# Performance work log

Measured on AMD Instinct MI355X. Metric: run time of the kernel, lower is better.

Reference implementation:

```python
import jax, jax.numpy as jnp
import numpy as np

N, E = 50000, 600000
D_IN, D_H, D_OUT, D_E = 128, 128, 128, 32


def setup_inputs() -> dict:
    key = jax.random.key(0)
    ks = jax.random.split(key, 20)
    s = 0.05
    inp = {
        "x": jax.random.normal(ks[0], (N, D_IN), dtype=jnp.float32),
        "edge_index": jax.random.randint(ks[1], (2, E), 0, N, dtype=jnp.int64),
        "edge_attr": jax.random.normal(ks[2], (E, D_E), dtype=jnp.float32),
        # layer 0 (GINEConv MLP + edge lin: edge_dim -> in_channels)
        "w1_0": jax.random.normal(ks[3], (D_IN, D_H), dtype=jnp.float32) * s,
        "b1_0": jnp.zeros((D_H,), jnp.float32),
        "w2_0": jax.random.normal(ks[4], (D_H, D_H), dtype=jnp.float32) * s,
        "b2_0": jnp.zeros((D_H,), jnp.float32),
        "we_0": jax.random.normal(ks[5], (D_E, D_IN), dtype=jnp.float32) * s,
        "be_0": jnp.zeros((D_IN,), jnp.float32),
        # layer 1 (edge lin: edge_dim -> hidden_channels)
        "w1_1": jax.random.normal(ks[6], (D_H, D_H), dtype=jnp.float32) * s,
        "b1_1": jnp.zeros((D_H,), jnp.float32),
        "w2_1": jax.random.normal(ks[7], (D_H, D_H), dtype=jnp.float32) * s,
        "b2_1": jnp.zeros((D_H,), jnp.float32),
        "we_1": jax.random.normal(ks[8], (D_E, D_H), dtype=jnp.float32) * s,
        "be_1": jnp.zeros((D_H,), jnp.float32),
        # output head
        "fc1_w": jax.random.normal(ks[9], (D_H, D_H), dtype=jnp.float32) * s,
        "fc1_b": jnp.zeros((D_H,), jnp.float32),
        "fc2_w": jax.random.normal(ks[10], (D_H, D_OUT), dtype=jnp.float32) * s,
        "fc2_b": jnp.zeros((D_OUT,), jnp.float32),
    }
    return inp


def _gine_layer(x, src, dst, edge_attr, we, be, w1, b1, w2, b2):
    # GINEConv (eps=0): out = MLP(x + sum_j ReLU(x_j + edge_lin(e_ij)))
    e_emb = edge_attr @ we + be                       # [E, d]
    msg = jax.nn.relu(x[src] + e_emb)                 # gather + message
    agg = jax.ops.segment_sum(msg, dst, num_segments=x.shape[0])  # scatter-add
    h = agg + x                                       # (1 + eps) * x, eps = 0
    return jnp.maximum(h @ w1 + b1, 0.0) @ w2 + b2    # 2-layer MLP


def reference(x, edge_index, edge_attr,
              w1_0, b1_0, w2_0, b2_0, we_0, be_0,
              w1_1, b1_1, w2_1, b2_1, we_1, be_1,
              fc1_w, fc1_b, fc2_w, fc2_b):
    src, dst = edge_index[0], edge_index[1]
    h = _gine_layer(x, src, dst, edge_attr, we_0, be_0, w1_0, b1_0, w2_0, b2_0)
    h = jax.nn.relu(h)  # activation (dropout=0 -> identity)
    h = _gine_layer(h, src, dst, edge_attr, we_1, be_1, w1_1, b1_1, w2_1, b2_1)
    h = jax.nn.relu(h)
    h = jax.nn.relu(h @ fc1_w + fc1_b)
    return h @ fc2_w + fc2_b
```

## Files before the change

kernel.cpp:

```cpp
#include <hip/hip_runtime.h>
#include <stdint.h>


#define ND 128
#define ED 32

typedef __attribute__((ext_vector_type(8))) short short8;
typedef __attribute__((ext_vector_type(4))) float f32x4;

__device__ inline unsigned short bf16_hi(float f) {
    union { float f; unsigned u; } v;
    v.f = f;
    return (unsigned short)(v.u >> 16);
}
__device__ inline float bf16_f(unsigned short h) {
    union { unsigned u; float f; } v;
    v.u = ((unsigned)h) << 16;
    return v.f;
}

__global__ __launch_bounds__(256) void zero_kernel(int* __restrict__ p, int n) {
    int i = blockIdx.x * blockDim.x + threadIdx.x;
    if (i < n) p[i] = 0;
}

__global__ __launch_bounds__(256) void hist_kernel(const int* __restrict__ ei,
                                                   int* __restrict__ counts, int E) {
    int i = blockIdx.x * blockDim.x + threadIdx.x;
    if (i < E) atomicAdd(&counts[ei[E + i]], 1);
}

__global__ __launch_bounds__(256) void bsum_kernel(const int* __restrict__ counts,
                                                   int* __restrict__ bsum, int N) {
    __shared__ int s[256];
    int t = threadIdx.x;
    int i = blockIdx.x * 256 + t;
    s[t] = (i < N) ? counts[i] : 0;
    __syncthreads();
#pragma unroll
    for (int off = 128; off > 0; off >>= 1) {
        if (t < off) s[t] += s[t + off];
        __syncthreads();
    }
    if (t == 0) bsum[blockIdx.x] = s[0];
}

__global__ __launch_bounds__(256) void scan_bsums(const int* __restrict__ bsum,
                                                  int* __restrict__ bofs,
                                                  int* __restrict__ row_start_N, int NB) {
    __shared__ int s[256];
    int t = threadIdx.x;
    int chunk = (NB + 255) >> 8;
    int lo = min(t * chunk, NB);
    int hi = min(lo + chunk, NB);
    int sum = 0;
    for (int i = lo; i < hi; ++i) sum += bsum[i];
    s[t] = sum;
    __syncthreads();
    for (int off = 1; off < 256; off <<= 1) {
        int v = (t >= off) ? s[t - off] : 0;
        __syncthreads();
        s[t] += v;
        __syncthreads();
    }
    int pre = (t == 0) ? 0 : s[t - 1];
    for (int i = lo; i < hi; ++i) {
        bofs[i] = pre;
        pre += bsum[i];
    }
    if (t == 255) *row_start_N = s[255];
}

__global__ __launch_bounds__(256) void expand_kernel(const int* __restrict__ counts,
                                                     const int* __restrict__ bofs,
                                                     int* __restrict__ row_start,
                                                     int* __restrict__ woff, int N) {
    __shared__ int s[256];
    int t = threadIdx.x;
    int i = blockIdx.x * 256 + t;
    int c = (i < N) ? counts[i] : 0;
    s[t] = c;
    __syncthreads();
    for (int off = 1; off < 256; off <<= 1) {
        int v = (t >= off) ? s[t - off] : 0;
        __syncthreads();
        s[t] += v;
        __syncthreads();
    }
    if (i < N) {
        int pre = bofs[blockIdx.x] + s[t] - c;
        row_start[i] = pre;
        woff[i] = pre;
    }
}

__global__ __launch_bounds__(256) void scatter_kernel(const int* __restrict__ ei,
                                                      int* __restrict__ woff,
                                                      int2* __restrict__ pack, int E) {
    int i = blockIdx.x * blockDim.x + threadIdx.x;
    if (i < E) {
        int d = ei[E + i];
        int p = atomicAdd(&woff[d], 1);
        pack[p] = make_int2(ei[i], i);
    }
}

__global__ __launch_bounds__(256) void wprep_kernel(
    const float* __restrict__ w0, const float* __restrict__ w1,
    const float* __restrict__ w2, const float* __restrict__ w3,
    const float* __restrict__ w4, const float* __restrict__ w5,
    unsigned short* __restrict__ hi, unsigned short* __restrict__ lo) {
    int t = blockIdx.x * blockDim.x + threadIdx.x;
    const float* W;
    switch (blockIdx.y) {
        case 0: W = w0; break;
        case 1: W = w1; break;
        case 2: W = w2; break;
        case 3: W = w3; break;
        case 4: W = w4; break;
        default: W = w5; break;
    }
    unsigned short* dh = hi + (size_t)blockIdx.y * 16384;
    unsigned short* dl = lo + (size_t)blockIdx.y * 16384;
    int c = t >> 6, l = t & 63;
    int nt = c >> 2, ks = c & 3;
    int n = nt * 16 + (l & 15);
    int kb = ks * 32 + ((l >> 4) << 3);
#pragma unroll
    for (int j = 0; j < 8; ++j) {
        float f = W[(size_t)(kb + j) * ND + n];
        unsigned short h = bf16_hi(f);
        dh[((size_t)c * 64 + l) * 8 + j] = h;
        dl[((size_t)c * 64 + l) * 8 + j] = bf16_hi(f - bf16_f(h));
    }
}

__global__ __launch_bounds__(256) void wprep_we(const float* __restrict__ w0,
                                                const float* __restrict__ w1,
                                                unsigned short* __restrict__ hi) {
    int t = threadIdx.x;
    int c = (blockIdx.x << 2) + (t >> 6);
    int l = t & 63;
    const float* W = blockIdx.y ? w1 : w0;
    unsigned short* dh = hi + (size_t)blockIdx.y * 4096;
    int n = c * 16 + (l & 15);
    int kb = (l >> 4) << 3;
#pragma unroll
    for (int j = 0; j < 8; ++j)
        dh[((size_t)c * 64 + l) * 8 + j] = bf16_hi(W[(size_t)(kb + j) * ND + n]);
}

__global__ __launch_bounds__(256) void xprep_kernel(const float* __restrict__ X,
                                                    const float* __restrict__ be,
                                                    unsigned short* __restrict__ xpk,
                                                    int N) {
    int t = blockIdx.x * 256 + threadIdx.x;
    int total = (N + 1) * 16;
    if (t >= total) return;
    int v = t >> 4, g = t & 15;
    short8 h, l;
    if (v < N) {
        const float4* p = (const float4*)(X + (size_t)v * ND + g * 8);
        float4 a0 = p[0], a1 = p[1];
        float f[8] = {a0.x, a0.y, a0.z, a0.w, a1.x, a1.y, a1.z, a1.w};
#pragma unroll
        for (int j = 0; j < 8; ++j) {
            float fv = f[j] + be[g * 8 + j];
            unsigned short hh = bf16_hi(fv);
            h[j] = (short)hh;
            l[j] = (short)bf16_hi(fv - bf16_f(hh));
        }
    } else {
#pragma unroll
        for (int j = 0; j < 8; ++j) {
            h[j] = (short)0xC6EA;
            l[j] = 0;
        }
    }
    unsigned short* dst = xpk + (size_t)t * 16;
    *(short8*)dst = h;
    *(short8*)(dst + 8) = l;
}

__global__ __launch_bounds__(256, 4) void agg_mfma(
    const float* __restrict__ xin, const float* __restrict__ edge_attr,
    const unsigned short* __restrict__ xpk, const unsigned short* __restrict__ bfh,
    const int* __restrict__ row_start, const int2* __restrict__ pack,
    float* __restrict__ hout, int N, int NW) {
    int lane = threadIdx.x & 63;
    int gw = (blockIdx.x * blockDim.x + threadIdx.x) >> 6;
    int m = lane & 15;
    int quad = lane >> 4;

    short8 bh[8];
#pragma unroll
    for (int nt = 0; nt < 8; ++nt)
        bh[nt] = *(const short8*)(bfh + ((size_t)nt * 64 + lane) * 8);

    short8 idf[2];
#pragma unroll
    for (int q = 0; q < 2; ++q)
#pragma unroll
        for (int j = 0; j < 8; ++j)
            idf[q][j] = (quad * 8 + j == q * 16 + m) ? (short)0x3F80 : (short)0;

    int col0 = quad * 32 + m;
    int col1 = col0 + 16;

    for (int v = gw; v < N; v += NW) {
        int beg = row_start[v];
        int end = row_start[v + 1];
        float res0 = xin[(size_t)v * ND + col0];
        float res1 = xin[(size_t)v * ND + col1];
        float part[8];
#pragma unroll
        for (int nt = 0; nt < 8; ++nt) part[nt] = 0.f;

        for (int base = beg; base < end; base += 16) {
            int rem = end - base;
            int mm = m < rem ? m : rem - 1;
            int2 pk = pack[base + mm];
            int s = m < rem ? pk.x : N;

            const unsigned short* xr = xpk + ((size_t)s * 16 + quad) * 16;
            short8 xh[4], xl[4];
#pragma unroll
            for (int kc = 0; kc < 4; ++kc) {
                xh[kc] = *(const short8*)(xr + kc * 64);
                xl[kc] = *(const short8*)(xr + kc * 64 + 8);
            }
            const float4* ar = (const float4*)(edge_attr + (size_t)pk.y * ED + quad * 8);
            float4 a0 = ar[0], a1 = ar[1];

            float af[8] = {a0.x, a0.y, a0.z, a0.w, a1.x, a1.y, a1.z, a1.w};
            short8 ah, al;
#pragma unroll
            for (int j = 0; j < 8; ++j) {
                unsigned short h = bf16_hi(af[j]);
                ah[j] = (short)h;
                al[j] = (short)bf16_hi(af[j] - bf16_f(h));
            }

#pragma unroll
            for (int nt = 0; nt < 8; ++nt) {
                f32x4 a = {0.f, 0.f, 0.f, 0.f};
                a = __builtin_amdgcn_mfma_f32_16x16x32_bf16(ah, bh[nt], a, 0, 0, 0);
                a = __builtin_amdgcn_mfma_f32_16x16x32_bf16(al, bh[nt], a, 0, 0, 0);
                a = __builtin_amdgcn_mfma_f32_16x16x32_bf16(xh[nt >> 1], idf[nt & 1], a,
                                                            0, 0, 0);
                a = __builtin_amdgcn_mfma_f32_16x16x32_bf16(xl[nt >> 1], idf[nt & 1], a,
                                                            0, 0, 0);
#pragma unroll
                for (int r = 0; r < 4; ++r)
                    part[nt] += fmaxf(a[r], 0.f);
            }
        }
#pragma unroll
        for (int nt = 0; nt < 8; ++nt) {
            float p = part[nt];
            p += __shfl_xor(p, 16, 64);
            p += __shfl_xor(p, 32, 64);
            part[nt] = p;
        }
        float o0 = quad == 0 ? part[0] : quad == 1 ? part[2] : quad == 2 ? part[4] : part[6];
        float o1 = quad == 0 ? part[1] : quad == 1 ? part[3] : quad == 2 ? part[5] : part[7];
        hout[(size_t)v * ND + col0] = res0 + o0;
        hout[(size_t)v * ND + col1] = res1 + o1;
    }
}

#define LP 132
__global__ __launch_bounds__(256, 4) void mlp2_mfma(
    const float* __restrict__ A,
    const unsigned short* __restrict__ w1h, const unsigned short* __restrict__ w1l,
    const float* __restrict__ b1,
    const unsigned short* __restrict__ w2h, const unsigned short* __restrict__ w2l,
    const float* __restrict__ b2,
    float* __restrict__ C, int N, int relu2) {
    __shared__ float tile[4][16 * LP];
    int lane = threadIdx.x & 63;
    int wave = threadIdx.x >> 6;
    int gw = blockIdx.x * 4 + wave;
    int m0 = gw * 16;
    if (m0 >= N) return;
    int m = lane & 15;
    int quad = lane >> 4;
    float* T = tile[wave];

    int row = m0 + m;
    bool rok = row < N;
    short8 ah[4], al[4];
#pragma unroll
    for (int ks = 0; ks < 4; ++ks) {
        float f[8];
        if (rok) {
            const float4* p = (const float4*)(A + (size_t)row * ND + ks * 32 + quad * 8);
            float4 a0 = p[0], a1 = p[1];
            f[0] = a0.x; f[1] = a0.y; f[2] = a0.z; f[3] = a0.w;
            f[4] = a1.x; f[5] = a1.y; f[6] = a1.z; f[7] = a1.w;
        } else {
#pragma unroll
            for (int j = 0; j < 8; ++j) f[j] = 0.f;
        }
#pragma unroll
        for (int j = 0; j < 8; ++j) {
            unsigned short hh = bf16_hi(f[j]);
            ah[ks][j] = (short)hh;
            al[ks][j] = (short)bf16_hi(f[j] - bf16_f(hh));
        }
    }

#pragma unroll
    for (int nt = 0; nt < 8; ++nt) {
        f32x4 acc = {0.f, 0.f, 0.f, 0.f};
#pragma unroll
        for (int ks = 0; ks < 4; ++ks) {
            size_t off = ((size_t)(nt * 4 + ks) * 64 + lane) * 8;
            short8 bh = *(const short8*)(w1h + off);
            short8 bl = *(const short8*)(w1l + off);
            acc = __builtin_amdgcn_mfma_f32_16x16x32_bf16(ah[ks], bh, acc, 0, 0, 0);
            acc = __builtin_amdgcn_mfma_f32_16x16x32_bf16(al[ks], bh, acc, 0, 0, 0);
            acc = __builtin_amdgcn_mfma_f32_16x16x32_bf16(ah[ks], bl, acc, 0, 0, 0);
        }
        float bv = b1[nt * 16 + m];
#pragma unroll
        for (int r = 0; r < 4; ++r) {
            float o = acc[r] + bv;
            o = o > 0.f ? o : 0.f;
            T[(quad * 4 + r) * LP + nt * 16 + m] = o;
        }
    }

    short8 ch[4], cl[4];
#pragma unroll
    for (int ks = 0; ks < 4; ++ks) {
        const float4* p = (const float4*)(T + m * LP + ks * 32 + quad * 8);
        float4 a0 = p[0], a1 = p[1];
        float f[8] = {a0.x, a0.y, a0.z, a0.w, a1.x, a1.y, a1.z, a1.w};
#pragma unroll
        for (int j = 0; j < 8; ++j) {
            unsigned short hh = bf16_hi(f[j]);
            ch[ks][j] = (short)hh;
            cl[ks][j] = (short)bf16_hi(f[j] - bf16_f(hh));
        }
    }

#pragma unroll
    for (int nt = 0; nt < 8; ++nt) {
        f32x4 acc = {0.f, 0.f, 0.f, 0.f};
#pragma unroll
        for (int ks = 0; ks < 4; ++ks) {
            size_t off = ((size_t)(nt * 4 + ks) * 64 + lane) * 8;
            short8 bh = *(const short8*)(w2h + off);
            short8 bl = *(const short8*)(w2l + off);
            acc = __builtin_amdgcn_mfma_f32_16x16x32_bf16(ch[ks], bh, acc, 0, 0, 0);
            acc = __builtin_amdgcn_mfma_f32_16x16x32_bf16(cl[ks], bh, acc, 0, 0, 0);
            acc = __builtin_amdgcn_mfma_f32_16x16x32_bf16(ch[ks], bl, acc, 0, 0, 0);
        }
        float bv = b2[nt * 16 + m];
#pragma unroll
        for (int r = 0; r < 4; ++r) {
            int rr = m0 + quad * 4 + r;
            if (rr < N) {
                float o = acc[r] + bv;
                if (relu2) o = o > 0.f ? o : 0.f;
                C[(size_t)rr * ND + nt * 16 + m] = o;
            }
        }
    }
}

extern "C" void kernel_launch(void* const* d_in, const int* in_sizes, int n_in,
                              void* d_out, int out_size, void* d_ws, size_t ws_size,
                              hipStream_t stream) {
    const float* x = (const float*)d_in[0];
    const int* ei = (const int*)d_in[1];
    const float* ea = (const float*)d_in[2];
    const float* w1_0 = (const float*)d_in[3];
    const float* b1_0 = (const float*)d_in[4];
    const float* w2_0 = (const float*)d_in[5];
    const float* b2_0 = (const float*)d_in[6];
    const float* we_0 = (const float*)d_in[7];
    const float* be_0 = (const float*)d_in[8];
    const float* w1_1 = (const float*)d_in[9];
    const float* b1_1 = (const float*)d_in[10];
    const float* w2_1 = (const float*)d_in[11];
    const float* b2_1 = (const float*)d_in[12];
    const float* we_1 = (const float*)d_in[13];
    const float* be_1 = (const float*)d_in[14];
    const float* fc1_w = (const float*)d_in[15];
    const float* fc1_b = (const float*)d_in[16];
    const float* fc2_w = (const float*)d_in[17];
    const float* fc2_b = (const float*)d_in[18];

    int N = in_sizes[0] / ND;
    int E = in_sizes[2] / ED;
    int NB = (N + 255) / 256;

    float* bufA = (float*)d_ws;
    int* counts = (int*)(bufA + (size_t)N * ND);
    int* row_start = counts + N;
    int* woff = row_start + (N + 1);
    int* bsum = woff + N;
    int* bofs = bsum + NB;
    int2* pack = (int2*)((((uintptr_t)(bofs + NB)) + 15) & ~(uintptr_t)15);
    unsigned short* wfh = (unsigned short*)(pack + E);
    unsigned short* wfl = wfh + 6 * 16384;
    unsigned short* weh = wfl + 6 * 16384;
    unsigned short* xpk = weh + 2 * 4096;
    float* out = (float*)d_out;

    zero_kernel<<<(N + 255) / 256, 256, 0, stream>>>(counts, N);
    hist_kernel<<<(E + 255) / 256, 256, 0, stream>>>(ei, counts, E);
    bsum_kernel<<<NB, 256, 0, stream>>>(counts, bsum, N);
    scan_bsums<<<1, 256, 0, stream>>>(bsum, bofs, row_start + N, NB);
    expand_kernel<<<NB, 256, 0, stream>>>(counts, bofs, row_start, woff, N);
    scatter_kernel<<<(E + 255) / 256, 256, 0, stream>>>(ei, woff, pack, E);
    wprep_kernel<<<dim3(8, 6), 256, 0, stream>>>(w1_0, w2_0, w1_1, w2_1, fc1_w, fc2_w,
                                                 wfh, wfl);
    wprep_we<<<dim3(2, 2), 256, 0, stream>>>(we_0, we_1, weh);

    const int NW = 8192;
    int gg = ((N + 15) / 16 + 3) / 4;
    int gx = ((N + 1) * 16 + 255) / 256;

    xprep_kernel<<<gx, 256, 0, stream>>>(x, be_0, xpk, N);
    agg_mfma<<<NW / 4, 256, 0, stream>>>(x, ea, xpk, weh, row_start, pack, out, N, NW);
    mlp2_mfma<<<gg, 256, 0, stream>>>(out, wfh + 0 * 16384, wfl + 0 * 16384, b1_0,
                                      wfh + 1 * 16384, wfl + 1 * 16384, b2_0, bufA, N, 1);

    xprep_kernel<<<gx, 256, 0, stream>>>(bufA, be_1, xpk, N);
    agg_mfma<<<NW / 4, 256, 0, stream>>>(bufA, ea, xpk, weh + 4096, row_start, pack, out,
                                         N, NW);
    mlp2_mfma<<<gg, 256, 0, stream>>>(out, wfh + 2 * 16384, wfl + 2 * 16384, b1_1,
                                      wfh + 3 * 16384, wfl + 3 * 16384, b2_1, bufA, N, 1);

    mlp2_mfma<<<gg, 256, 0, stream>>>(bufA, wfh + 4 * 16384, wfl + 4 * 16384, fc1_b,
                                      wfh + 5 * 16384, wfl + 5 * 16384, fc2_b, out, N, 0);
}
```

Baseline: 564.4 us.

## Balance aggregation work by edge count with contiguous node ranges per wave

Adds a kernel that binary-searches the CSR row offsets so each of 4096 waves gets a contiguous node range with roughly equal edge counts, replacing the strided node-per-wave loop over 8192 waves. Inside the aggregation loop, the next 16-edge pack entry is prefetched one chunk ahead, and beg is carried from the previous node instead of reloaded. The aim is better load balance and hidden gather latency, at the cost of an extra small launch and half as many waves.

```diff
diff --git a/kernel.cpp b/kernel.cpp
--- a/kernel.cpp
+++ b/kernel.cpp
@@ -105,6 +105,22 @@
     }
 }
 
+__global__ __launch_bounds__(256) void wrange_kernel(const int* __restrict__ row_start,
+                                                     int* __restrict__ wstart,
+                                                     int N, int E, int NW) {
+    int w = blockIdx.x * 256 + threadIdx.x;
+    if (w > NW) return;
+    if (w == 0) { wstart[0] = 0; return; }
+    if (w == NW) { wstart[NW] = N; return; }
+    int T = (int)((long long)w * E / NW);
+    int lo = 0, hi = N - 1;
+    while (lo < hi) {
+        int mid = (lo + hi) >> 1;
+        if (row_start[mid + 1] > T) hi = mid; else lo = mid + 1;
+    }
+    wstart[w] = lo;
+}
+
 __global__ __launch_bounds__(256) void wprep_kernel(
     const float* __restrict__ w0, const float* __restrict__ w1,
     const float* __restrict__ w2, const float* __restrict__ w3,
@@ -185,8 +201,8 @@
 __global__ __launch_bounds__(256, 4) void agg_mfma(
     const float* __restrict__ xin, const float* __restrict__ edge_attr,
     const unsigned short* __restrict__ xpk, const unsigned short* __restrict__ bfh,
-    const int* __restrict__ row_start, const int2* __restrict__ pack,
-    float* __restrict__ hout, int N, int NW) {
+    const int* __restrict__ row_start, const int* __restrict__ wstart,
+    const int2* __restrict__ pack, float* __restrict__ hout, int N, int E) {
     int lane = threadIdx.x & 63;
     int gw = (blockIdx.x * blockDim.x + threadIdx.x) >> 6;
     int m = lane & 15;
@@ -207,8 +223,14 @@
     int col0 = quad * 32 + m;
     int col1 = col0 + 16;
 
-    for (int v = gw; v < N; v += NW) {
-        int beg = row_start[v];
+    int v_lo = wstart[gw];
+    int v_hi = wstart[gw + 1];
+    if (v_lo >= v_hi) return;
+
+    int beg = row_start[v_lo];
+    int2 pk2 = pack[min(beg + m, E - 1)];
+
+    for (int v = v_lo; v < v_hi; ++v) {
         int end = row_start[v + 1];
         float res0 = xin[(size_t)v * ND + col0];
         float res1 = xin[(size_t)v * ND + col1];
@@ -217,10 +239,12 @@
         for (int nt = 0; nt < 8; ++nt) part[nt] = 0.f;
 
         for (int base = beg; base < end; base += 16) {
+            int2 pk = pk2;
+            int nxt = (base + 16 < end) ? base + 16 : end;
+            pk2 = pack[min(nxt + m, E - 1)];
+
             int rem = end - base;
-            int mm = m < rem ? m : rem - 1;
-            int2 pk = pack[base + mm];
-            int s = m < rem ? pk.x : N;
+            int s = (m < rem) ? pk.x : N;
 
             const unsigned short* xr = xpk + ((size_t)s * 16 + quad) * 16;
             short8 xh[4], xl[4];
@@ -266,6 +290,7 @@
         float o1 = quad == 0 ? part[1] : quad == 1 ? part[3] : quad == 2 ? part[5] : part[7];
         hout[(size_t)v * ND + col0] = res0 + o0;
         hout[(size_t)v * ND + col1] = res1 + o1;
+        beg = end;
     }
 }
 
@@ -396,6 +421,7 @@
     int N = in_sizes[0] / ND;
     int E = in_sizes[2] / ED;
     int NB = (N + 255) / 256;
+    const int NW = 4096;
 
     float* bufA = (float*)d_ws;
     int* counts = (int*)(bufA + (size_t)N * ND);
@@ -403,7 +429,8 @@
     int* woff = row_start + (N + 1);
     int* bsum = woff + N;
     int* bofs = bsum + NB;
-    int2* pack = (int2*)((((uintptr_t)(bofs + NB)) + 15) & ~(uintptr_t)15);
+    int* wstart = bofs + NB;
+    int2* pack = (int2*)((((uintptr_t)(wstart + NW + 1)) + 15) & ~(uintptr_t)15);
     unsigned short* wfh = (unsigned short*)(pack + E);
     unsigned short* wfl = wfh + 6 * 16384;
     unsigned short* weh = wfl + 6 * 16384;
@@ -416,22 +443,23 @@
     scan_bsums<<<1, 256, 0, stream>>>(bsum, bofs, row_start + N, NB);
     expand_kernel<<<NB, 256, 0, stream>>>(counts, bofs, row_start, woff, N);
     scatter_kernel<<<(E + 255) / 256, 256, 0, stream>>>(ei, woff, pack, E);
+    wrange_kernel<<<(NW + 1 + 255) / 256, 256, 0, stream>>>(row_start, wstart, N, E, NW);
     wprep_kernel<<<dim3(8, 6), 256, 0, stream>>>(w1_0, w2_0, w1_1, w2_1, fc1_w, fc2_w,
                                                  wfh, wfl);
     wprep_we<<<dim3(2, 2), 256, 0, stream>>>(we_0, we_1, weh);
 
-    const int NW = 8192;
     int gg = ((N + 15) / 16 + 3) / 4;
     int gx = ((N + 1) * 16 + 255) / 256;
 
     xprep_kernel<<<gx, 256, 0, stream>>>(x, be_0, xpk, N);
-    agg_mfma<<<NW / 4, 256, 0, stream>>>(x, ea, xpk, weh, row_start, pack, out, N, NW);
+    agg_mfma<<<NW / 4, 256, 0, stream>>>(x, ea, xpk, weh, row_start, wstart, pack, out,
+                                         N, E);
     mlp2_mfma<<<gg, 256, 0, stream>>>(out, wfh + 0 * 16384, wfl + 0 * 16384, b1_0,
                                       wfh + 1 * 16384, wfl + 1 * 16384, b2_0, bufA, N, 1);
 
     xprep_kernel<<<gx, 256, 0, stream>>>(bufA, be_1, xpk, N);
-    agg_mfma<<<NW / 4, 256, 0, stream>>>(bufA, ea, xpk, weh + 4096, row_start, pack, out,
-                                         N, NW);
+    agg_mfma<<<NW / 4, 256, 0, stream>>>(bufA, ea, xpk, weh + 4096, row_start, wstart,
+                                         pack, out, N, E);
     mlp2_mfma<<<gg, 256, 0, stream>>>(out, wfh + 2 * 16384, wfl + 2 * 16384, b1_1,
                                       wfh + 3 * 16384, wfl + 3 * 16384, b2_1, bufA, N, 1);
 
```

New measurement: 492.3 us. 12.8% less time.

## Balance aggregation over 16-edge chunks and software-pipeline gathers with double buffering

Applied to the files above, without the earlier changes.

Builds a per-node chunk list (16-edge chunks) with extra scan kernels, then splits the chunks evenly across waves by binary search, so each wave handles a contiguous, balanced set of chunks instead of striding over nodes. The aggregation loop is double-buffered: metadata and gathers for the next chunks are issued before the current chunk's MFMA work, and outputs are flushed when the node changes. Edge-weight fragments move from registers into LDS, and the wave count drops from 8192 to 4096. In exchange there are several extra small setup kernels, and register pressure rises from holding two gather buffers.

```diff
diff --git a/kernel.cpp b/kernel.cpp
--- a/kernel.cpp
+++ b/kernel.cpp
@@ -18,6 +18,8 @@
     v.u = ((unsigned)h) << 16;
     return v.f;
 }
+
+__device__ inline int cc_of(int d) { return d ? (d + 15) >> 4 : 1; }
 
 __global__ __launch_bounds__(256) void zero_kernel(int* __restrict__ p, int n) {
     int i = blockIdx.x * blockDim.x + threadIdx.x;
@@ -45,9 +47,24 @@
     if (t == 0) bsum[blockIdx.x] = s[0];
 }
 
+__global__ __launch_bounds__(256) void cbsum_kernel(const int* __restrict__ counts,
+                                                    int* __restrict__ bsum, int N) {
+    __shared__ int s[256];
+    int t = threadIdx.x;
+    int i = blockIdx.x * 256 + t;
+    s[t] = (i < N) ? cc_of(counts[i]) : 0;
+    __syncthreads();
+#pragma unroll
+    for (int off = 128; off > 0; off >>= 1) {
+        if (t < off) s[t] += s[t + off];
+        __syncthreads();
+    }
+    if (t == 0) bsum[blockIdx.x] = s[0];
+}
+
 __global__ __launch_bounds__(256) void scan_bsums(const int* __restrict__ bsum,
                                                   int* __restrict__ bofs,
-                                                  int* __restrict__ row_start_N, int NB) {
+                                                  int* __restrict__ total_out, int NB) {
     __shared__ int s[256];
     int t = threadIdx.x;
     int chunk = (NB + 255) >> 8;
@@ -68,7 +85,7 @@
         bofs[i] = pre;
         pre += bsum[i];
     }
-    if (t == 255) *row_start_N = s[255];
+    if (t == 255) *total_out = s[255];
 }
 
 __global__ __launch_bounds__(256) void expand_kernel(const int* __restrict__ counts,
@@ -94,6 +111,24 @@
     }
 }
 
+__global__ __launch_bounds__(256) void cexpand_kernel(const int* __restrict__ counts,
+                                                      const int* __restrict__ bofs,
+                                                      int* __restrict__ cofs, int N) {
+    __shared__ int s[256];
+    int t = threadIdx.x;
+    int i = blockIdx.x * 256 + t;
+    int c = (i < N) ? cc_of(counts[i]) : 0;
+    s[t] = c;
+    __syncthreads();
+    for (int off = 1; off < 256; off <<= 1) {
+        int v = (t >= off) ? s[t - off] : 0;
+        __syncthreads();
+        s[t] += v;
+        __syncthreads();
+    }
+    if (i < N) cofs[i] = bofs[blockIdx.x] + s[t] - c;
+}
+
 __global__ __launch_bounds__(256) void scatter_kernel(const int* __restrict__ ei,
                                                       int* __restrict__ woff,
                                                       int2* __restrict__ pack, int E) {
@@ -103,6 +138,39 @@
         int p = atomicAdd(&woff[d], 1);
         pack[p] = make_int2(ei[i], i);
     }
+}
+
+__global__ __launch_bounds__(256) void cfill_kernel(const int* __restrict__ row_start,
+                                                    const int* __restrict__ cofs,
+                                                    int2* __restrict__ cmeta, int N) {
+    int v = blockIdx.x * 256 + threadIdx.x;
+    if (v >= N) return;
+    int beg = row_start[v], end = row_start[v + 1];
+    int deg = end - beg;
+    int nc = cc_of(deg);
+    int co = cofs[v];
+    for (int j = 0; j < nc; ++j) {
+        int rem = deg - j * 16;
+        rem = rem > 16 ? 16 : (rem < 0 ? 0 : rem);
+        cmeta[co + j] = make_int2(beg + j * 16, (v << 5) | rem);
+    }
+}
+
+__global__ __launch_bounds__(256) void cwrange_kernel(const int* __restrict__ cofs,
+                                                      int* __restrict__ cws,
+                                                      int N, int NW) {
+    int w = blockIdx.x * 256 + threadIdx.x;
+    if (w > NW) return;
+    int NC = cofs[N];
+    if (w == 0) { cws[0] = 0; return; }
+    if (w == NW) { cws[NW] = NC; return; }
+    long long T = (long long)w * NC / NW;
+    int lo = 0, hi = N - 1;
+    while (lo < hi) {
+        int mid = (lo + hi) >> 1;
+        if (cofs[mid + 1] > T) hi = mid; else lo = mid + 1;
+    }
+    cws[w] = cofs[lo];
 }
 
 __global__ __launch_bounds__(256) void wprep_kernel(
@@ -182,20 +250,91 @@
     *(short8*)(dst + 8) = l;
 }
 
+#define GATHER(S, MM, PKK)                                                      \
+    {                                                                           \
+        int rem_ = (MM).y & 31;                                                 \
+        int s_ = (m < rem_) ? (PKK).x : N;                                      \
+        const unsigned short* xr_ = xpk + ((size_t)s_ * 16 + quad) * 16;        \
+        _Pragma("unroll") for (int kc = 0; kc < 4; ++kc) {                      \
+            xh_##S[kc] = *(const short8*)(xr_ + kc * 64);                       \
+            xl_##S[kc] = *(const short8*)(xr_ + kc * 64 + 8);                   \
+        }                                                                       \
+        const float4* ar_ =                                                     \
+            (const float4*)(edge_attr + (size_t)(PKK).y * ED + quad * 8);       \
+        ea_##S[0] = ar_[0];                                                     \
+        ea_##S[1] = ar_[1];                                                     \
+    }
+
+#define COMPUTE(S)                                                              \
+    {                                                                           \
+        float af_[8] = {ea_##S[0].x, ea_##S[0].y, ea_##S[0].z, ea_##S[0].w,     \
+                        ea_##S[1].x, ea_##S[1].y, ea_##S[1].z, ea_##S[1].w};    \
+        short8 ah_, al_;                                                        \
+        _Pragma("unroll") for (int j = 0; j < 8; ++j) {                         \
+            unsigned short h_ = bf16_hi(af_[j]);                                \
+            ah_[j] = (short)h_;                                                 \
+            al_[j] = (short)bf16_hi(af_[j] - bf16_f(h_));                       \
+        }                                                                       \
+        _Pragma("unroll") for (int nt = 0; nt < 8; ++nt) {                      \
+            short8 bh_ = *(const short8*)(bhs + ((size_t)nt * 64 + lane) * 8);  \
+            f32x4 a_ = {0.f, 0.f, 0.f, 0.f};                                    \
+            a_ = __builtin_amdgcn_mfma_f32_16x16x32_bf16(ah_, bh_, a_, 0, 0, 0);\
+            a_ = __builtin_amdgcn_mfma_f32_16x16x32_bf16(al_, bh_, a_, 0, 0, 0);\
+            a_ = __builtin_amdgcn_mfma_f32_16x16x32_bf16(xh_##S[nt >> 1],       \
+                                                         idf[nt & 1], a_, 0, 0, 0); \
+            a_ = __builtin_amdgcn_mfma_f32_16x16x32_bf16(xl_##S[nt >> 1],       \
+                                                         idf[nt & 1], a_, 0, 0, 0); \
+            _Pragma("unroll") for (int r = 0; r < 4; ++r)                       \
+                part[nt] += fmaxf(a_[r], 0.f);                                  \
+        }                                                                       \
+    }
+
+#define FLUSHCHK(C_, NODEN_)                                                    \
+    if ((C_) == cap || (NODEN_) != curv) {                                      \
+        _Pragma("unroll") for (int nt = 0; nt < 8; ++nt) {                      \
+            float p_ = part[nt];                                                \
+            p_ += __shfl_xor(p_, 16, 64);                                       \
+            p_ += __shfl_xor(p_, 32, 64);                                       \
+            part[nt] = p_;                                                      \
+        }                                                                       \
+        float o0_ = quad == 0 ? part[0] : quad == 1 ? part[2]                   \
+                  : quad == 2 ? part[4] : part[6];                              \
+        float o1_ = quad == 0 ? part[1] : quad == 1 ? part[3]                   \
+                  : quad == 2 ? part[5] : part[7];                              \
+        hout[(size_t)curv * ND + col0] = res0 + o0_;                            \
+        hout[(size_t)curv * ND + col1] = res1 + o1_;                            \
+        if ((C_) != cap) {                                                      \
+            curv = (NODEN_);                                                    \
+            res0 = xin[(size_t)curv * ND + col0];                               \
+            res1 = xin[(size_t)curv * ND + col1];                               \
+            _Pragma("unroll") for (int nt = 0; nt < 8; ++nt) part[nt] = 0.f;    \
+        }                                                                       \
+    }
+
 __global__ __launch_bounds__(256, 4) void agg_mfma(
     const float* __restrict__ xin, const float* __restrict__ edge_attr,
     const unsigned short* __restrict__ xpk, const unsigned short* __restrict__ bfh,
-    const int* __restrict__ row_start, const int2* __restrict__ pack,
-    float* __restrict__ hout, int N, int NW) {
+    const int* __restrict__ cws, const int2* __restrict__ cmeta,
+    const int2* __restrict__ pack, float* __restrict__ hout, int N, int E) {
+    __shared__ unsigned short bhs[8 * 64 * 8];
     int lane = threadIdx.x & 63;
-    int gw = (blockIdx.x * blockDim.x + threadIdx.x) >> 6;
+    int wave = threadIdx.x >> 6;
     int m = lane & 15;
     int quad = lane >> 4;
 
-    short8 bh[8];
-#pragma unroll
-    for (int nt = 0; nt < 8; ++nt)
-        bh[nt] = *(const short8*)(bfh + ((size_t)nt * 64 + lane) * 8);
+    {
+        int nt0 = wave * 2;
+        *(short8*)(bhs + ((size_t)nt0 * 64 + lane) * 8) =
+            *(const short8*)(bfh + ((size_t)nt0 * 64 + lane) * 8);
+        *(short8*)(bhs + ((size_t)(nt0 + 1) * 64 + lane) * 8) =
+            *(const short8*)(bfh + ((size_t)(nt0 + 1) * 64 + lane) * 8);
+    }
+    __syncthreads();
+
+    int gw = (blockIdx.x * blockDim.x + threadIdx.x) >> 6;
+    int c_lo = cws[gw], c_hi = cws[gw + 1];
+    if (c_lo >= c_hi) return;
+    int cap = c_hi - 1;
 
     short8 idf[2];
 #pragma unroll
@@ -207,65 +346,49 @@
     int col0 = quad * 32 + m;
     int col1 = col0 + 16;
 
-    for (int v = gw; v < N; v += NW) {
-        int beg = row_start[v];
-        int end = row_start[v + 1];
-        float res0 = xin[(size_t)v * ND + col0];
-        float res1 = xin[(size_t)v * ND + col1];
-        float part[8];
-#pragma unroll
-        for (int nt = 0; nt < 8; ++nt) part[nt] = 0.f;
-
-        for (int base = beg; base < end; base += 16) {
-            int rem = end - base;
-            int mm = m < rem ? m : rem - 1;
-            int2 pk = pack[base + mm];
-            int s = m < rem ? pk.x : N;
-
-            const unsigned short* xr = xpk + ((size_t)s * 16 + quad) * 16;
-            short8 xh[4], xl[4];
-#pragma unroll
-            for (int kc = 0; kc < 4; ++kc) {
-                xh[kc] = *(const short8*)(xr + kc * 64);
-                xl[kc] = *(const short8*)(xr + kc * 64 + 8);
-            }
-            const float4* ar = (const float4*)(edge_attr + (size_t)pk.y * ED + quad * 8);
-            float4 a0 = ar[0], a1 = ar[1];
-
-            float af[8] = {a0.x, a0.y, a0.z, a0.w, a1.x, a1.y, a1.z, a1.w};
-            short8 ah, al;
-#pragma unroll
-            for (int j = 0; j < 8; ++j) {
-                unsigned short h = bf16_hi(af[j]);
-                ah[j] = (short)h;
-                al[j] = (short)bf16_hi(af[j] - bf16_f(h));
-            }
-
-#pragma unroll
-            for (int nt = 0; nt < 8; ++nt) {
-                f32x4 a = {0.f, 0.f, 0.f, 0.f};
-                a = __builtin_amdgcn_mfma_f32_16x16x32_bf16(ah, bh[nt], a, 0, 0, 0);
-                a = __builtin_amdgcn_mfma_f32_16x16x32_bf16(al, bh[nt], a, 0, 0, 0);
-                a = __builtin_amdgcn_mfma_f32_16x16x32_bf16(xh[nt >> 1], idf[nt & 1], a,
-                                                            0, 0, 0);
-                a = __builtin_amdgcn_mfma_f32_16x16x32_bf16(xl[nt >> 1], idf[nt & 1], a,
-                                                            0, 0, 0);
-#pragma unroll
-                for (int r = 0; r < 4; ++r)
-                    part[nt] += fmaxf(a[r], 0.f);
-            }
-        }
-#pragma unroll
-        for (int nt = 0; nt < 8; ++nt) {
-            float p = part[nt];
-            p += __shfl_xor(p, 16, 64);
-            p += __shfl_xor(p, 32, 64);
-            part[nt] = p;
-        }
-        float o0 = quad == 0 ? part[0] : quad == 1 ? part[2] : quad == 2 ? part[4] : part[6];
-        float o1 = quad == 0 ? part[1] : quad == 1 ? part[3] : quad == 2 ? part[5] : part[7];
-        hout[(size_t)v * ND + col0] = res0 + o0;
-        hout[(size_t)v * ND + col1] = res1 + o1;
+    int2 m0 = cmeta[c_lo];
+    int2 m1 = cmeta[min(c_lo + 1, cap)];
+    int2 m2 = cmeta[min(c_lo + 2, cap)];
+    int2 pk0 = pack[min(m0.x + m, E - 1)];
+    int2 pk1 = pack[min(m1.x + m, E - 1)];
+    int2 pk2 = pack[min(m2.x + m, E - 1)];
+
+    short8 xh_a[4], xl_a[4]; float4 ea_a[2];
+    short8 xh_b[4], xl_b[4]; float4 ea_b[2];
+
+    GATHER(a, m0, pk0);
+    int curv = m0.y >> 5;
+    float res0 = xin[(size_t)curv * ND + col0];
+    float res1 = xin[(size_t)curv * ND + col1];
+    float part[8];
+#pragma unroll
+    for (int nt = 0; nt < 8; ++nt) part[nt] = 0.f;
+
+    int c = c_lo;
+    while (true) {
+        {
+            int noden = m1.y >> 5;
+            GATHER(b, m1, pk1);
+            m1 = m2; pk1 = pk2;
+            m2 = cmeta[min(c + 3, cap)];
+            pk2 = pack[min(m2.x + m, E - 1)];
+            COMPUTE(a);
+            FLUSHCHK(c, noden);
+        }
+        ++c;
+        if (c >= c_hi) break;
+
+        {
+            int noden = m1.y >> 5;
+            GATHER(a, m1, pk1);
+            m1 = m2; pk1 = pk2;
+            m2 = cmeta[min(c + 3, cap)];
+            pk2 = pack[min(m2.x + m, E - 1)];
+            COMPUTE(b);
+            FLUSHCHK(c, noden);
+        }
+        ++c;
+        if (c >= c_hi) break;
     }
 }
 
@@ -396,6 +519,8 @@
     int N = in_sizes[0] / ND;
     int E = in_sizes[2] / ED;
     int NB = (N + 255) / 256;
+    const int NW = 4096;
+    int NCMAX = N + E / 16 + 16;
 
     float* bufA = (float*)d_ws;
     int* counts = (int*)(bufA + (size_t)N * ND);
@@ -403,7 +528,12 @@
     int* woff = row_start + (N + 1);
     int* bsum = woff + N;
     int* bofs = bsum + NB;
-    int2* pack = (int2*)((((uintptr_t)(bofs + NB)) + 15) & ~(uintptr_t)15);
+    int* bsum2 = bofs + NB;
+    int* bofs2 = bsum2 + NB;
+    int* cofs = bofs2 + NB;
+    int* cws = cofs + (N + 1);
+    int2* cmeta = (int2*)((((uintptr_t)(cws + NW + 1)) + 15) & ~(uintptr_t)15);
+    int2* pack = cmeta + NCMAX;
     unsigned short* wfh = (unsigned short*)(pack + E);
     unsigned short* wfl = wfh + 6 * 16384;
     unsigned short* weh = wfl + 6 * 16384;
@@ -416,22 +546,26 @@
     scan_bsums<<<1, 256, 0, stream>>>(bsum, bofs, row_start + N, NB);
     expand_kernel<<<NB, 256, 0, stream>>>(counts, bofs, row_start, woff, N);
     scatter_kernel<<<(E + 255) / 256, 256, 0, stream>>>(ei, woff, pack, E);
+    cbsum_kernel<<<NB, 256, 0, stream>>>(counts, bsum2, N);
+    scan_bsums<<<1, 256, 0, stream>>>(bsum2, bofs2, cofs + N, NB);
+    cexpand_kernel<<<NB, 256, 0, stream>>>(counts, bofs2, cofs, N);
+    cfill_kernel<<<(N + 255) / 256, 256, 0, stream>>>(row_start, cofs, cmeta, N);
+    cwrange_kernel<<<(NW + 1 + 255) / 256, 256, 0, stream>>>(cofs, cws, N, NW);
     wprep_kernel<<<dim3(8, 6), 256, 0, stream>>>(w1_0, w2_0, w1_1, w2_1, fc1_w, fc2_w,
                                                  wfh, wfl);
     wprep_we<<<dim3(2, 2), 256, 0, stream>>>(we_0, we_1, weh);
 
-    const int NW = 8192;
     int gg = ((N + 15) / 16 + 3) / 4;
     int gx = ((N + 1) * 16 + 255) / 256;
 
     xprep_kernel<<<gx, 256, 0, stream>>>(x, be_0, xpk, N);
-    agg_mfma<<<NW / 4, 256, 0, stream>>>(x, ea, xpk, weh, row_start, pack, out, N, NW);
+    agg_mfma<<<NW / 4, 256, 0, stream>>>(x, ea, xpk, weh, cws, cmeta, pack, out, N, E);
     mlp2_mfma<<<gg, 256, 0, stream>>>(out, wfh + 0 * 16384, wfl + 0 * 16384, b1_0,
                                       wfh + 1 * 16384, wfl + 1 * 16384, b2_0, bufA, N, 1);
 
     xprep_kernel<<<gx, 256, 0, stream>>>(bufA, be_1, xpk, N);
-    agg_mfma<<<NW / 4, 256, 0, stream>>>(bufA, ea, xpk, weh + 4096, row_start, pack, out,
-                                         N, NW);
+    agg_mfma<<<NW / 4, 256, 0, stream>>>(bufA, ea, xpk, weh + 4096, cws, cmeta, pack, out,
+                                         N, E);
     mlp2_mfma<<<gg, 256, 0, stream>>>(out, wfh + 2 * 16384, wfl + 2 * 16384, b1_1,
                                       wfh + 3 * 16384, wfl + 3 * 16384, b2_1, bufA, N, 1);
 
```

Measured after the change: 637.7 us. 13.0% more time.
